# Optimization experiments

Measured on AMD Instinct MI355X. Metric: run time of the kernel, lower is better.

## Reference

```python
import jax, jax.numpy as jnp
import numpy as np
import math

N_HEADS = 16
D_MODEL = 1024
DK = D_MODEL // N_HEADS
B, S = 2, 2048


def setup_inputs() -> dict:
    key = jax.random.key(0)
    ks = jax.random.split(key, 11)
    scale_in = 1.0 / math.sqrt(D_MODEL)
    scale_o = 1.0 / math.sqrt(N_HEADS * DK)
    return {
        "query": jax.random.normal(ks[0], (B, S, D_MODEL), jnp.float32),
        "key": jax.random.normal(ks[1], (B, S, D_MODEL), jnp.float32),
        "value": jax.random.normal(ks[2], (B, S, D_MODEL), jnp.float32),
        # stacked per-head projection weights [H, d_model, dk], biases [H, dk]
        "Wq": jax.random.normal(ks[3], (N_HEADS, D_MODEL, DK), jnp.float32) * scale_in,
        "bq": jax.random.normal(ks[4], (N_HEADS, DK), jnp.float32) * scale_in,
        "Wk": jax.random.normal(ks[5], (N_HEADS, D_MODEL, DK), jnp.float32) * scale_in,
        "bk": jax.random.normal(ks[6], (N_HEADS, DK), jnp.float32) * scale_in,
        "Wv": jax.random.normal(ks[7], (N_HEADS, D_MODEL, DK), jnp.float32) * scale_in,
        "bv": jax.random.normal(ks[8], (N_HEADS, DK), jnp.float32) * scale_in,
        "Wo": jax.random.normal(ks[9], (N_HEADS * DK, D_MODEL), jnp.float32) * scale_o,
        "bo": jax.random.normal(ks[10], (D_MODEL,), jnp.float32) * scale_o,
    }


def reference(query, key, value, Wq, bq, Wk, bk, Wv, bv, Wo, bo):
    # Per-head linear projections, vectorized over heads: [B,H,S,dk]
    q = jnp.einsum("bsd,hdk->bhsk", query, Wq) + bq[None, :, None, :]
    k = jnp.einsum("bsd,hdk->bhsk", key, Wk) + bk[None, :, None, :]
    v = jnp.einsum("bsd,hdk->bhsk", value, Wv) + bv[None, :, None, :]
    # Scaled dot-product scores [B,H,S,S]
    scores = jnp.einsum("bhsk,bhtk->bhst", q, k) / jnp.sqrt(jnp.asarray(DK, q.dtype))
    # FAITHFUL to source: nn.Softmax(dim=0) -> softmax over the BATCH axis
    attn = jax.nn.softmax(scores, axis=0)
    out = jnp.einsum("bhst,bhtk->bhsk", attn, v)  # [B,H,S,dk]
    # concat heads along feature dim (torch.cat dim=2)
    concat = out.transpose(0, 2, 1, 3).reshape(query.shape[0], query.shape[1], N_HEADS * DK)
    return concat @ Wo + bo
```

## Files before the change

### kernel.cpp

```cpp
#include <hip/hip_runtime.h>
#include <hip/hip_bf16.h>

#define B_ 2
#define S_ 2048
#define D_ 1024
#define H_ 16
#define DK_ 64
#define BS_ (B_ * S_)

typedef unsigned int u32;
typedef unsigned short u16;
typedef __attribute__((ext_vector_type(8))) short bf16x8;
typedef __attribute__((ext_vector_type(4))) float f32x4;

typedef const __attribute__((address_space(1))) void glb_cv;
typedef __attribute__((address_space(3))) void lds_v;

__device__ __forceinline__ void async_cp16(const void* g, void* l) {
    __builtin_amdgcn_global_load_lds((glb_cv*)g, (lds_v*)l, 16, 0, 0);
}

__device__ __forceinline__ float bf2f(u16 v) {
    union { u32 u; float f; } c; c.u = ((u32)v) << 16; return c.f;
}
__device__ __forceinline__ u16 f2bf(float f) {
    union { float f; u32 u; } c; c.f = f;
    u32 u = c.u;
    return (u16)((u + 0x7fffu + ((u >> 16) & 1u)) >> 16);
}
__device__ __forceinline__ u32 pack2(float a, float b) {
    return (u32)f2bf(a) | ((u32)f2bf(b) << 16);
}
__device__ __forceinline__ u32 packtr(float lo, float hi) {
    union { float f; u32 u; } a, b; a.f = lo; b.f = hi;
    return __builtin_amdgcn_perm(b.u, a.u, 0x07060302u);
}
__device__ __forceinline__ int sw64(int r, int c8) { return (((c8) + (r)) & 7) * 8; }

struct PrepArgs {
    const float* W[4]; u16* WT[4];
    const float* X[3]; u16* XB[3];
};
__global__ __launch_bounds__(256) void prep(PrepArgs a)
{
    const int id = blockIdx.x;
    const int tid = threadIdx.x;
    if (id >= 1024) {
        const int cid = id - 1024;
        const int z = cid >> 11;
        const size_t base = (size_t)(cid & 2047) * 2048 + tid * 8;
        const float* X = a.X[z];
        float4 x0 = *(const float4*)(X + base);
        float4 x1 = *(const float4*)(X + base + 4);
        uint4 o;
        o.x = pack2(x0.x, x0.y); o.y = pack2(x0.z, x0.w);
        o.z = pack2(x1.x, x1.y); o.w = pack2(x1.z, x1.w);
        *(uint4*)(a.XB[z] + base) = o;
        return;
    }
    __shared__ __attribute__((aligned(16))) u16 T[64][72];
    const int z = id >> 8;
    const int rem = id & 255;
    const float* W = a.W[z];
    u16* WT = a.WT[z];
    const int headMode = (z < 3) ? 1 : 0;
    const int k0 = (rem >> 4) * 64;
    const int n0 = (rem & 15) * 64;
    const int kr = tid >> 4;
    const int n4 = (tid & 15) * 4;
    #pragma unroll
    for (int pass = 0; pass < 4; ++pass) {
        int kk = k0 + pass * 16 + kr;
        const float* p = headMode
            ? (W + (size_t)((n0 + n4) >> 6) * (1024 * 64) + kk * 64 + ((n0 + n4) & 63))
            : (W + (size_t)kk * 1024 + n0 + n4);
        float4 v = *(const float4*)p;
        int krel = pass * 16 + kr;
        T[n4 + 0][krel] = f2bf(v.x);
        T[n4 + 1][krel] = f2bf(v.y);
        T[n4 + 2][krel] = f2bf(v.z);
        T[n4 + 3][krel] = f2bf(v.w);
    }
    __syncthreads();
    const int nr = tid >> 2;
    const int kq = (tid & 3) * 16;
    uint4 o0 = *(const uint4*)&T[nr][kq];
    uint4 o1 = *(const uint4*)&T[nr][kq + 8];
    u16* q = WT + (size_t)(n0 + nr) * 1024 + k0 + kq;
    *(uint4*)q = o0;
    *(uint4*)(q + 8) = o1;
}

struct ProjArgs {
    const u16* X[3];
    const u16* W[3];
    const float* bias[3];
    u16* Y[3];
};
__global__ __launch_bounds__(256) void proj3(ProjArgs pa)
{
    __shared__ __attribute__((aligned(16))) u16 As[2][128][32];
    __shared__ __attribute__((aligned(16))) u16 Bs[2][128][32];
    const int z = blockIdx.z;
    const u16* X = pa.X[z];
    const u16* WT = pa.W[z];
    const float* bias = pa.bias[z];
    u16* Y = pa.Y[z];
    const int neg = (z == 1);

    const int tid = threadIdx.x;
    const int lane = tid & 63;
    const int wave = tid >> 6;
    const int quad = lane >> 4;
    const int l16 = lane & 15;
    const int m0 = blockIdx.x * 128;
    const int n0 = blockIdx.y * 128;
    const int wm = (wave & 1) * 64, wn = (wave >> 1) * 64;

    f32x4 acc[4][4] = {};

    for (int k0 = 0; k0 < 1024; k0 += 64) {
        __syncthreads();
        #pragma unroll
        for (int ks = 0; ks < 2; ++ks)
            #pragma unroll
            for (int call = 0; call < 2; ++call) {
                const int c = tid + call * 256;
                const int row = c >> 2, cc = (c & 3) * 8;
                char* la = (char*)&As[ks][0][0] + (size_t)(c & ~63) * 16;
                async_cp16(X + (size_t)(m0 + row) * 1024 + k0 + ks * 32 + cc, la);
                char* lb = (char*)&Bs[ks][0][0] + (size_t)(c & ~63) * 16;
                async_cp16(WT + (size_t)(n0 + row) * 1024 + k0 + ks * 32 + cc, lb);
            }
        __syncthreads();

        #pragma unroll
        for (int ks = 0; ks < 2; ++ks) {
            bf16x8 af[4], bfr[4];
            #pragma unroll
            for (int mt = 0; mt < 4; ++mt)
                af[mt] = *(const bf16x8*)&As[ks][wm + mt * 16 + l16][quad * 8];
            #pragma unroll
            for (int nt = 0; nt < 4; ++nt)
                bfr[nt] = *(const bf16x8*)&Bs[ks][wn + nt * 16 + l16][quad * 8];
            #pragma unroll
            for (int mt = 0; mt < 4; ++mt)
                #pragma unroll
                for (int nt = 0; nt < 4; ++nt)
                    acc[mt][nt] = __builtin_amdgcn_mfma_f32_16x16x32_bf16(
                        af[mt], bfr[nt], acc[mt][nt], 0, 0, 0);
        }
    }

    if (z == 2) {
        #pragma unroll
        for (int nt = 0; nt < 4; ++nt) {
            const int col = n0 + wn + nt * 16 + l16;
            const float bv = bias[col];
            u16* vrow = Y + ((size_t)(col >> 6) * 64 + (col & 63)) * 2048;
            #pragma unroll
            for (int mt = 0; mt < 4; ++mt) {
                const int row = m0 + wm + mt * 16 + quad * 4;
                const size_t boff = (size_t)(row >> 11) * (16 * 64 * 2048);
                const int t = row & 2047;
                uint2 w;
                w.x = pack2(acc[mt][nt][0] + bv, acc[mt][nt][1] + bv);
                w.y = pack2(acc[mt][nt][2] + bv, acc[mt][nt][3] + bv);
                *(uint2*)(vrow + boff + t) = w;
            }
        }
        return;
    }

    #pragma unroll
    for (int nt = 0; nt < 4; ++nt) {
        const int col = n0 + wn + nt * 16 + l16;
        const float bv = bias[col];
        #pragma unroll
        for (int mt = 0; mt < 4; ++mt) {
            #pragma unroll
            for (int r = 0; r < 4; ++r) {
                const int row = m0 + wm + mt * 16 + quad * 4 + r;
                float v = acc[mt][nt][r] + bv;
                if (neg && row >= 2048) v = -v;
                Y[(size_t)row * 1024 + col] = f2bf(v);
            }
        }
    }
}

__global__ __launch_bounds__(256) void gemm_out(
    const u16* __restrict__ P0, const u16* __restrict__ P1,
    const float* __restrict__ csP,
    const u16* __restrict__ WT, const float* __restrict__ bias,
    float* __restrict__ Y)
{
    __shared__ __attribute__((aligned(16))) u16 Aa[128][32];
    __shared__ __attribute__((aligned(16))) u16 Ab[128][32];
    __shared__ __attribute__((aligned(16))) u16 Bs[64][32];
    __shared__ __attribute__((aligned(16))) float csL[1024];

    const int tid = threadIdx.x;
    const int lane = tid & 63;
    const int wave = tid >> 6;
    const int quad = lane >> 4;
    const int l16 = lane & 15;
    const int m0 = blockIdx.x * 128;
    const int n0 = blockIdx.y * 64;
    const int wm = (wave & 1) * 64, wn = (wave >> 1) * 32;
    const bool hiB = (m0 >= 2048);

    {
        const int t4 = tid * 4;
        float4 c0 = *(const float4*)(csP + t4);
        float4 c1 = *(const float4*)(csP + 1024 + t4);
        csL[t4 + 0] = c0.x + c1.x;
        csL[t4 + 1] = c0.y + c1.y;
        csL[t4 + 2] = c0.z + c1.z;
        csL[t4 + 3] = c0.w + c1.w;
    }

    f32x4 acc[4][2] = {};

    for (int k0 = 0; k0 < 1024; k0 += 32) {
        __syncthreads();
        #pragma unroll
        for (int call = 0; call < 2; ++call) {
            const int c = tid + call * 256;
            const int row = c >> 2, cc = (c & 3) * 8;
            char* la = (char*)&Aa[0][0] + (size_t)(c & ~63) * 16;
            async_cp16(P0 + (size_t)(m0 + row) * 1024 + k0 + cc, la);
            char* lb = (char*)&Ab[0][0] + (size_t)(c & ~63) * 16;
            async_cp16(P1 + (size_t)(m0 + row) * 1024 + k0 + cc, lb);
        }
        {
            const int c = tid;
            const int row = c >> 2, cc = (c & 3) * 8;
            char* lb = (char*)&Bs[0][0] + (size_t)(c & ~63) * 16;
            async_cp16(WT + (size_t)(n0 + row) * 1024 + k0 + cc, lb);
        }
        __syncthreads();

        float4 cs0, cs1;
        if (hiB) {
            cs0 = *(const float4*)&csL[k0 + quad * 8];
            cs1 = *(const float4*)&csL[k0 + quad * 8 + 4];
        }
        bf16x8 af[4], bfr[2];
        #pragma unroll
        for (int mt = 0; mt < 4; ++mt) {
            bf16x8 aa = *(const bf16x8*)&Aa[wm + mt * 16 + l16][quad * 8];
            bf16x8 ab = *(const bf16x8*)&Ab[wm + mt * 16 + l16][quad * 8];
            float v[8];
            #pragma unroll
            for (int jj = 0; jj < 8; ++jj)
                v[jj] = bf2f((u16)aa[jj]) + bf2f((u16)ab[jj]);
            if (hiB) {
                v[0] = cs0.x - v[0]; v[1] = cs0.y - v[1];
                v[2] = cs0.z - v[2]; v[3] = cs0.w - v[3];
                v[4] = cs1.x - v[4]; v[5] = cs1.y - v[5];
                v[6] = cs1.z - v[6]; v[7] = cs1.w - v[7];
            }
            u32* rp = (u32*)&af[mt];
            rp[0] = pack2(v[0], v[1]); rp[1] = pack2(v[2], v[3]);
            rp[2] = pack2(v[4], v[5]); rp[3] = pack2(v[6], v[7]);
        }
        #pragma unroll
        for (int nt = 0; nt < 2; ++nt)
            bfr[nt] = *(const bf16x8*)&Bs[wn + nt * 16 + l16][quad * 8];
        #pragma unroll
        for (int mt = 0; mt < 4; ++mt)
            #pragma unroll
            for (int nt = 0; nt < 2; ++nt)
                acc[mt][nt] = __builtin_amdgcn_mfma_f32_16x16x32_bf16(
                    af[mt], bfr[nt], acc[mt][nt], 0, 0, 0);
    }

    #pragma unroll
    for (int nt = 0; nt < 2; ++nt) {
        const int col = n0 + wn + nt * 16 + l16;
        const float bv = bias[col];
        #pragma unroll
        for (int mt = 0; mt < 4; ++mt) {
            #pragma unroll
            for (int r = 0; r < 4; ++r) {
                const int row = m0 + wm + mt * 16 + quad * 4 + r;
                Y[(size_t)row * 1024 + col] = acc[mt][nt][r] + bv;
            }
        }
    }
}

__global__ __launch_bounds__(256) void attn_mfma(
    const u16* __restrict__ Qb, const u16* __restrict__ Kb,
    const u16* __restrict__ VT, float* __restrict__ csP,
    u16* __restrict__ P0, u16* __restrict__ P1)
{
    __shared__ __attribute__((aligned(16))) u16 Ks[2][2][64][64];
    __shared__ __attribute__((aligned(16))) u16 Vs[2][2][64][64];
    __shared__ __attribute__((aligned(16))) u16 Ps[128][64];

    const int id = blockIdx.x;
    const int xcd = id & 7;
    const int rj = id >> 3;
    const int h = xcd * 2 + (rj >> 5);
    const int half = (rj >> 4) & 1;
    const int st = rj & 15;
    const int s0 = st * 128;
    const int tbase = half * 1024;
    u16* Pout = half ? P1 : P0;

    const int tid = threadIdx.x;
    const int lane = tid & 63;
    const int wave = tid >> 6;
    const int quad = lane >> 4;
    const int l16 = lane & 15;
    const int sr8 = lane >> 3;
    const int sc8 = lane & 7;

    auto stage = [&](int buf, int t0) {
        #pragma unroll
        for (int c = 0; c < 4; ++c) {
            const int kc = c * 4 + wave;
            const int bb = kc >> 3, row0 = (kc & 7) * 8;
            const int rr = row0 + sr8;
            const int cg = (sc8 - rr) & 7;
            async_cp16(Kb + (size_t)(bb * S_ + tbase + t0 + rr) * 1024 + h * 64 + cg * 8,
                       &Ks[buf][bb][row0][0]);
            async_cp16(VT + ((size_t)(bb * H_ + h) * 64 + rr) * 2048 + tbase + t0 + cg * 8,
                       &Vs[buf][bb][row0][0]);
        }
    };

    bf16x8 qf[2][2][2];
    #pragma unroll
    for (int sg = 0; sg < 2; ++sg)
        #pragma unroll
        for (int b = 0; b < 2; ++b)
            #pragma unroll
            for (int ks = 0; ks < 2; ++ks)
                qf[sg][b][ks] = *(const bf16x8*)(Qb
                    + (size_t)(b * S_ + s0 + wave * 32 + sg * 16 + l16) * 1024
                    + h * 64 + ks * 32 + quad * 8);

    f32x4 O0[2][4] = {}, T1[2][4] = {};
    float cacc = 0.f;

    stage(0, 0);
    __syncthreads();
    int cur = 0;
    for (int t0 = 0; t0 < 1024; t0 += 64) {
        if (t0 + 64 < 1024) stage(cur ^ 1, t0 + 64);

        f32x4 dacc[2][4] = {};
        __builtin_amdgcn_s_setprio(1);
        #pragma unroll
        for (int mt = 0; mt < 4; ++mt) {
            const int kr = mt * 16 + l16;
            #pragma unroll
            for (int ks = 0; ks < 2; ++ks) {
                bf16x8 k0f = *(const bf16x8*)&Ks[cur][0][kr][sw64(kr, ks * 4 + quad)];
                bf16x8 k1f = *(const bf16x8*)&Ks[cur][1][kr][sw64(kr, ks * 4 + quad)];
                #pragma unroll
                for (int sg = 0; sg < 2; ++sg) {
                    dacc[sg][mt] = __builtin_amdgcn_mfma_f32_16x16x32_bf16(
                        k0f, qf[sg][0][ks], dacc[sg][mt], 0, 0, 0);
                    dacc[sg][mt] = __builtin_amdgcn_mfma_f32_16x16x32_bf16(
                        k1f, qf[sg][1][ks], dacc[sg][mt], 0, 0, 0);
                }
            }
        }
        __builtin_amdgcn_s_setprio(0);

        #pragma unroll
        for (int sg = 0; sg < 2; ++sg) {
            const int pr = wave * 32 + sg * 16 + l16;
            #pragma unroll
            for (int mt = 0; mt < 4; ++mt) {
                float p[4];
                #pragma unroll
                for (int rr = 0; rr < 4; ++rr) {
                    float e = __expf(dacc[sg][mt][rr] * -0.125f);
                    p[rr] = __builtin_amdgcn_rcpf(1.0f + e);
                }
                uint2 w;
                w.x = packtr(p[0], p[1]);
                w.y = packtr(p[2], p[3]);
                const int c8 = 2 * mt + (quad >> 1);
                *(uint2*)&Ps[pr][sw64(pr, c8) + (quad & 1) * 4] = w;
            }
        }

        if (st == 0) {
            const int dk = tid >> 2, tp = tid & 3;
            bf16x8 vA = *(const bf16x8*)&Vs[cur][1][dk][sw64(dk, tp * 2)];
            bf16x8 vB = *(const bf16x8*)&Vs[cur][1][dk][sw64(dk, tp * 2 + 1)];
            #pragma unroll
            for (int jj = 0; jj < 8; ++jj)
                cacc += bf2f((u16)vA[jj]) + bf2f((u16)vB[jj]);
        }

        bf16x8 pf[2][2];
        #pragma unroll
        for (int sg = 0; sg < 2; ++sg) {
            const int pr = wave * 32 + sg * 16 + l16;
            pf[sg][0] = *(const bf16x8*)&Ps[pr][sw64(pr, quad)];
            pf[sg][1] = *(const bf16x8*)&Ps[pr][sw64(pr, 4 + quad)];
        }
        __builtin_amdgcn_s_setprio(1);
        #pragma unroll
        for (int nt = 0; nt < 4; ++nt) {
            const int vr = nt * 16 + l16;
            bf16x8 v00 = *(const bf16x8*)&Vs[cur][0][vr][sw64(vr, quad)];
            bf16x8 v01 = *(const bf16x8*)&Vs[cur][0][vr][sw64(vr, 4 + quad)];
            bf16x8 v10 = *(const bf16x8*)&Vs[cur][1][vr][sw64(vr, quad)];
            bf16x8 v11 = *(const bf16x8*)&Vs[cur][1][vr][sw64(vr, 4 + quad)];
            #pragma unroll
            for (int sg = 0; sg < 2; ++sg) {
                O0[sg][nt] = __builtin_amdgcn_mfma_f32_16x16x32_bf16(pf[sg][0], v00, O0[sg][nt], 0, 0, 0);
                O0[sg][nt] = __builtin_amdgcn_mfma_f32_16x16x32_bf16(pf[sg][1], v01, O0[sg][nt], 0, 0, 0);
                T1[sg][nt] = __builtin_amdgcn_mfma_f32_16x16x32_bf16(pf[sg][0], v10, T1[sg][nt], 0, 0, 0);
                T1[sg][nt] = __builtin_amdgcn_mfma_f32_16x16x32_bf16(pf[sg][1], v11, T1[sg][nt], 0, 0, 0);
            }
        }
        __builtin_amdgcn_s_setprio(0);
        __syncthreads();
        cur ^= 1;
    }

    #pragma unroll
    for (int sg = 0; sg < 2; ++sg)
        #pragma unroll
        for (int nt = 0; nt < 4; ++nt) {
            const int dk = nt * 16 + l16;
            #pragma unroll
            for (int rr = 0; rr < 4; ++rr) {
                const int s = s0 + wave * 32 + sg * 16 + quad * 4 + rr;
                Pout[(size_t)(0 * S_ + s) * 1024 + h * 64 + dk] = f2bf(O0[sg][nt][rr]);
                Pout[(size_t)(1 * S_ + s) * 1024 + h * 64 + dk] = f2bf(T1[sg][nt][rr]);
            }
        }

    if (st == 0) {
        cacc += __shfl_xor(cacc, 1);
        cacc += __shfl_xor(cacc, 2);
        if ((tid & 3) == 0)
            csP[half * 1024 + h * 64 + (tid >> 2)] = cacc;
    }
}

extern "C" void kernel_launch(void* const* d_in, const int* in_sizes, int n_in,
                              void* d_out, int out_size, void* d_ws, size_t ws_size,
                              hipStream_t stream) {
    const float* q  = (const float*)d_in[0];
    const float* k  = (const float*)d_in[1];
    const float* v  = (const float*)d_in[2];
    const float* Wq = (const float*)d_in[3];
    const float* bq = (const float*)d_in[4];
    const float* Wk = (const float*)d_in[5];
    const float* bk = (const float*)d_in[6];
    const float* Wv = (const float*)d_in[7];
    const float* bv = (const float*)d_in[8];
    const float* Wo = (const float*)d_in[9];
    const float* bo = (const float*)d_in[10];

    char* ws = (char*)d_ws;
    const size_t MB = 1024 * 1024;
    u16* Xq  = (u16*)(ws);
    float* csP = (float*)(ws);
    u16* WqT = (u16*)(ws + 8  * MB);
    u16* WkT = (u16*)(ws + 10 * MB);
    u16* WvT = (u16*)(ws + 12 * MB);
    u16* WoT = (u16*)(ws + 14 * MB);
    u16* Qp  = (u16*)(ws + 16 * MB);
    u16* Kp  = (u16*)(ws + 24 * MB);
    u16* VTv = (u16*)(ws + 32 * MB);
    u16* Xk  = (u16*)(ws + 40 * MB);
    u16* Pb  = (u16*)(ws + 40 * MB);
    u16* Xv  = (u16*)(ws + 48 * MB);
    u16* Pa  = (u16*)(ws + 48 * MB);

    dim3 blk(256);

    PrepArgs pr;
    pr.W[0] = Wq; pr.W[1] = Wk; pr.W[2] = Wv; pr.W[3] = Wo;
    pr.WT[0] = WqT; pr.WT[1] = WkT; pr.WT[2] = WvT; pr.WT[3] = WoT;
    pr.X[0] = q; pr.X[1] = k; pr.X[2] = v;
    pr.XB[0] = Xq; pr.XB[1] = Xk; pr.XB[2] = Xv;
    prep<<<dim3(1024 + 6144), blk, 0, stream>>>(pr);

    ProjArgs pa;
    pa.X[0] = Xq; pa.X[1] = Xk; pa.X[2] = Xv;
    pa.W[0] = WqT; pa.W[1] = WkT; pa.W[2] = WvT;
    pa.bias[0] = bq; pa.bias[1] = bk; pa.bias[2] = bv;
    pa.Y[0] = Qp; pa.Y[1] = Kp; pa.Y[2] = VTv;
    proj3<<<dim3(32, 8, 3), blk, 0, stream>>>(pa);

    attn_mfma<<<dim3(512), blk, 0, stream>>>(Qp, Kp, VTv, csP, Pa, Pb);
    gemm_out<<<dim3(32, 16), blk, 0, stream>>>(Pa, Pb, csP, WoT, bo, (float*)d_out);
}
```

Before: 249.1 us.

## Split attention key range three ways and single-buffer K/V to raise occupancy

The attention kernel now splits the key axis into three chunks (704/704/640 keys) instead of two, launching 768 blocks instead of 512. The output GEMM sums three partial buffers and three column-sum partials. K/V staging drops from double to single buffering, with K and V loads issued separately, to cut LDS use and allow 3 blocks per CU via launch bounds. This trades prefetch overlap and extra partial-buffer traffic in gemm_out for more parallelism and occupancy on the 256-CU device.

Result: slower. 256.6 us (+3.0%).

```diff
diff --git a/kernel.cpp b/kernel.cpp
--- a/kernel.cpp
+++ b/kernel.cpp
@@ -191,12 +191,13 @@
 
 __global__ __launch_bounds__(256) void gemm_out(
     const u16* __restrict__ P0, const u16* __restrict__ P1,
-    const float* __restrict__ csP,
+    const u16* __restrict__ P2, const float* __restrict__ csP,
     const u16* __restrict__ WT, const float* __restrict__ bias,
     float* __restrict__ Y)
 {
     __shared__ __attribute__((aligned(16))) u16 Aa[128][32];
     __shared__ __attribute__((aligned(16))) u16 Ab[128][32];
+    __shared__ __attribute__((aligned(16))) u16 Ac[128][32];
     __shared__ __attribute__((aligned(16))) u16 Bs[64][32];
     __shared__ __attribute__((aligned(16))) float csL[1024];
 
@@ -214,10 +215,11 @@
         const int t4 = tid * 4;
         float4 c0 = *(const float4*)(csP + t4);
         float4 c1 = *(const float4*)(csP + 1024 + t4);
-        csL[t4 + 0] = c0.x + c1.x;
-        csL[t4 + 1] = c0.y + c1.y;
-        csL[t4 + 2] = c0.z + c1.z;
-        csL[t4 + 3] = c0.w + c1.w;
+        float4 c2 = *(const float4*)(csP + 2048 + t4);
+        csL[t4 + 0] = c0.x + c1.x + c2.x;
+        csL[t4 + 1] = c0.y + c1.y + c2.y;
+        csL[t4 + 2] = c0.z + c1.z + c2.z;
+        csL[t4 + 3] = c0.w + c1.w + c2.w;
     }
 
     f32x4 acc[4][2] = {};
@@ -232,6 +234,8 @@
             async_cp16(P0 + (size_t)(m0 + row) * 1024 + k0 + cc, la);
             char* lb = (char*)&Ab[0][0] + (size_t)(c & ~63) * 16;
             async_cp16(P1 + (size_t)(m0 + row) * 1024 + k0 + cc, lb);
+            char* lc = (char*)&Ac[0][0] + (size_t)(c & ~63) * 16;
+            async_cp16(P2 + (size_t)(m0 + row) * 1024 + k0 + cc, lc);
         }
         {
             const int c = tid;
@@ -251,10 +255,11 @@
         for (int mt = 0; mt < 4; ++mt) {
             bf16x8 aa = *(const bf16x8*)&Aa[wm + mt * 16 + l16][quad * 8];
             bf16x8 ab = *(const bf16x8*)&Ab[wm + mt * 16 + l16][quad * 8];
+            bf16x8 ac = *(const bf16x8*)&Ac[wm + mt * 16 + l16][quad * 8];
             float v[8];
             #pragma unroll
             for (int jj = 0; jj < 8; ++jj)
-                v[jj] = bf2f((u16)aa[jj]) + bf2f((u16)ab[jj]);
+                v[jj] = bf2f((u16)aa[jj]) + bf2f((u16)ab[jj]) + bf2f((u16)ac[jj]);
             if (hiB) {
                 v[0] = cs0.x - v[0]; v[1] = cs0.y - v[1];
                 v[2] = cs0.z - v[2]; v[3] = cs0.w - v[3];
@@ -291,24 +296,26 @@
     }
 }
 
-__global__ __launch_bounds__(256) void attn_mfma(
+__global__ __launch_bounds__(256, 3) void attn_mfma(
     const u16* __restrict__ Qb, const u16* __restrict__ Kb,
     const u16* __restrict__ VT, float* __restrict__ csP,
-    u16* __restrict__ P0, u16* __restrict__ P1)
+    u16* __restrict__ P0, u16* __restrict__ P1, u16* __restrict__ P2)
 {
-    __shared__ __attribute__((aligned(16))) u16 Ks[2][2][64][64];
-    __shared__ __attribute__((aligned(16))) u16 Vs[2][2][64][64];
+    __shared__ __attribute__((aligned(16))) u16 Ks[2][64][64];
+    __shared__ __attribute__((aligned(16))) u16 Vs[2][64][64];
     __shared__ __attribute__((aligned(16))) u16 Ps[128][64];
 
     const int id = blockIdx.x;
     const int xcd = id & 7;
-    const int rj = id >> 3;
-    const int h = xcd * 2 + (rj >> 5);
-    const int half = (rj >> 4) & 1;
-    const int st = rj & 15;
+    const int j = id >> 3;
+    const int h = xcd * 2 + (j & 1);
+    const int r = j >> 1;
+    const int st = r & 15;
+    const int spl = r >> 4;
     const int s0 = st * 128;
-    const int tbase = half * 1024;
-    u16* Pout = half ? P1 : P0;
+    const int tstart = spl * 704;
+    const int ntile = (spl == 2) ? 10 : 11;
+    u16* Pout = (spl == 0) ? P0 : (spl == 1) ? P1 : P2;
 
     const int tid = threadIdx.x;
     const int lane = tid & 63;
@@ -318,17 +325,26 @@
     const int sr8 = lane >> 3;
     const int sc8 = lane & 7;
 
-    auto stage = [&](int buf, int t0) {
+    auto stageK = [&](int t0) {
         #pragma unroll
         for (int c = 0; c < 4; ++c) {
             const int kc = c * 4 + wave;
             const int bb = kc >> 3, row0 = (kc & 7) * 8;
             const int rr = row0 + sr8;
             const int cg = (sc8 - rr) & 7;
-            async_cp16(Kb + (size_t)(bb * S_ + tbase + t0 + rr) * 1024 + h * 64 + cg * 8,
-                       &Ks[buf][bb][row0][0]);
-            async_cp16(VT + ((size_t)(bb * H_ + h) * 64 + rr) * 2048 + tbase + t0 + cg * 8,
-                       &Vs[buf][bb][row0][0]);
+            async_cp16(Kb + (size_t)(bb * S_ + t0 + rr) * 1024 + h * 64 + cg * 8,
+                       &Ks[bb][row0][0]);
+        }
+    };
+    auto stageV = [&](int t0) {
+        #pragma unroll
+        for (int c = 0; c < 4; ++c) {
+            const int kc = c * 4 + wave;
+            const int bb = kc >> 3, row0 = (kc & 7) * 8;
+            const int rr = row0 + sr8;
+            const int cg = (sc8 - rr) & 7;
+            async_cp16(VT + ((size_t)(bb * H_ + h) * 64 + rr) * 2048 + t0 + cg * 8,
+                       &Vs[bb][row0][0]);
         }
     };
 
@@ -346,11 +362,11 @@
     f32x4 O0[2][4] = {}, T1[2][4] = {};
     float cacc = 0.f;
 
-    stage(0, 0);
+    stageK(tstart);
     __syncthreads();
-    int cur = 0;
-    for (int t0 = 0; t0 < 1024; t0 += 64) {
-        if (t0 + 64 < 1024) stage(cur ^ 1, t0 + 64);
+    for (int i = 0; i < ntile; ++i) {
+        const int t0 = tstart + i * 64;
+        stageV(t0);
 
         f32x4 dacc[2][4] = {};
         __builtin_amdgcn_s_setprio(1);
@@ -359,8 +375,8 @@
             const int kr = mt * 16 + l16;
             #pragma unroll
             for (int ks = 0; ks < 2; ++ks) {
-                bf16x8 k0f = *(const bf16x8*)&Ks[cur][0][kr][sw64(kr, ks * 4 + quad)];
-                bf16x8 k1f = *(const bf16x8*)&Ks[cur][1][kr][sw64(kr, ks * 4 + quad)];
+                bf16x8 k0f = *(const bf16x8*)&Ks[0][kr][sw64(kr, ks * 4 + quad)];
+                bf16x8 k1f = *(const bf16x8*)&Ks[1][kr][sw64(kr, ks * 4 + quad)];
                 #pragma unroll
                 for (int sg = 0; sg < 2; ++sg) {
                     dacc[sg][mt] = __builtin_amdgcn_mfma_f32_16x16x32_bf16(
@@ -391,10 +407,14 @@
             }
         }
 
+        __syncthreads();
+
+        if (i + 1 < ntile) stageK(t0 + 64);
+
         if (st == 0) {
             const int dk = tid >> 2, tp = tid & 3;
-            bf16x8 vA = *(const bf16x8*)&Vs[cur][1][dk][sw64(dk, tp * 2)];
-            bf16x8 vB = *(const bf16x8*)&Vs[cur][1][dk][sw64(dk, tp * 2 + 1)];
+            bf16x8 vA = *(const bf16x8*)&Vs[1][dk][sw64(dk, tp * 2)];
+            bf16x8 vB = *(const bf16x8*)&Vs[1][dk][sw64(dk, tp * 2 + 1)];
             #pragma unroll
             for (int jj = 0; jj < 8; ++jj)
                 cacc += bf2f((u16)vA[jj]) + bf2f((u16)vB[jj]);
@@ -411,10 +431,10 @@
         #pragma unroll
         for (int nt = 0; nt < 4; ++nt) {
             const int vr = nt * 16 + l16;
-            bf16x8 v00 = *(const bf16x8*)&Vs[cur][0][vr][sw64(vr, quad)];
-            bf16x8 v01 = *(const bf16x8*)&Vs[cur][0][vr][sw64(vr, 4 + quad)];
-            bf16x8 v10 = *(const bf16x8*)&Vs[cur][1][vr][sw64(vr, quad)];
-            bf16x8 v11 = *(const bf16x8*)&Vs[cur][1][vr][sw64(vr, 4 + quad)];
+            bf16x8 v00 = *(const bf16x8*)&Vs[0][vr][sw64(vr, quad)];
+            bf16x8 v01 = *(const bf16x8*)&Vs[0][vr][sw64(vr, 4 + quad)];
+            bf16x8 v10 = *(const bf16x8*)&Vs[1][vr][sw64(vr, quad)];
+            bf16x8 v11 = *(const bf16x8*)&Vs[1][vr][sw64(vr, 4 + quad)];
             #pragma unroll
             for (int sg = 0; sg < 2; ++sg) {
                 O0[sg][nt] = __builtin_amdgcn_mfma_f32_16x16x32_bf16(pf[sg][0], v00, O0[sg][nt], 0, 0, 0);
@@ -425,7 +445,6 @@
         }
         __builtin_amdgcn_s_setprio(0);
         __syncthreads();
-        cur ^= 1;
     }
 
     #pragma unroll
@@ -445,7 +464,7 @@
         cacc += __shfl_xor(cacc, 1);
         cacc += __shfl_xor(cacc, 2);
         if ((tid & 3) == 0)
-            csP[half * 1024 + h * 64 + (tid >> 2)] = cacc;
+            csP[spl * 1024 + h * 64 + (tid >> 2)] = cacc;
     }
 }
 
@@ -467,8 +486,9 @@
     char* ws = (char*)d_ws;
     const size_t MB = 1024 * 1024;
     u16* Xq  = (u16*)(ws);
-    float* csP = (float*)(ws);
+    u16* Pa  = (u16*)(ws);
     u16* WqT = (u16*)(ws + 8  * MB);
+    float* csP = (float*)(ws + 8 * MB);
     u16* WkT = (u16*)(ws + 10 * MB);
     u16* WvT = (u16*)(ws + 12 * MB);
     u16* WoT = (u16*)(ws + 14 * MB);
@@ -478,7 +498,7 @@
     u16* Xk  = (u16*)(ws + 40 * MB);
     u16* Pb  = (u16*)(ws + 40 * MB);
     u16* Xv  = (u16*)(ws + 48 * MB);
-    u16* Pa  = (u16*)(ws + 48 * MB);
+    u16* Pc  = (u16*)(ws + 48 * MB);
 
     dim3 blk(256);
 
@@ -496,6 +516,6 @@
     pa.Y[0] = Qp; pa.Y[1] = Kp; pa.Y[2] = VTv;
     proj3<<<dim3(32, 8, 3), blk, 0, stream>>>(pa);
 
-    attn_mfma<<<dim3(512), blk, 0, stream>>>(Qp, Kp, VTv, csP, Pa, Pb);
-    gemm_out<<<dim3(32, 16), blk, 0, stream>>>(Pa, Pb, csP, WoT, bo, (float*)d_out);
-}
+    attn_mfma<<<dim3(768), blk, 0, stream>>>(Qp, Kp, VTv, csP, Pa, Pb, Pc);
+    gemm_out<<<dim3(32, 16), blk, 0, stream>>>(Pa, Pb, Pc, csP, WoT, bo, (float*)d_out);
+}
```
